# Kernel optimization log

Hardware: AMD Instinct MI355X
Metric: run time of the kernel (lower is better)

Reference implementation:

```python
import jax, jax.numpy as jnp
import numpy as np

PAD, CLS, SEP, UNK = 0, 1, 2, 3
VOCAB, DIM, LATENT = 30000, 768, 5000
B, L, C = 16, 1024, 8


def setup_inputs() -> dict:
    key = jax.random.key(0)
    k1, k2, k3 = jax.random.split(key, 3)
    x = jax.random.randint(k1, (B, L, C), 0, VOCAB, dtype=jnp.int64)
    char_emb = jax.random.normal(k2, (VOCAB, DIM), dtype=jnp.float32)
    latent_mat = jax.random.normal(k3, (LATENT, DIM), dtype=jnp.float32) * (LATENT ** -0.5)
    return {"x": x, "char_emb": char_emb, "latent_mat": latent_mat}


def reference(x, char_emb, latent_mat):
    b, l, c = x.shape
    chars = x.reshape(-1, c)                       # (N, C)
    embs = char_emb[chars]                         # (N, C, D) gather
    pad_mask = chars == PAD                        # (N, C)
    embs = jnp.where(pad_mask[..., None], 0.0, embs)
    summed = embs.sum(axis=1)                      # (N, D)
    counts = jnp.clip((~pad_mask).sum(axis=-1), 1, None)  # (N,)
    lang_emb = jnp.tanh(summed / counts[:, None].astype(summed.dtype))  # (N, D)

    # soft codebook attention: matmul -> softmax -> matmul
    scores = jnp.einsum('nd,kd->nk', lang_emb, latent_mat)   # (N, LATENT)
    dist = jax.nn.softmax(scores, axis=-1)
    latent_emb = jnp.einsum('nk,kd->nd', dist, latent_mat)    # (N, D)
    sde = lang_emb + latent_emb

    # special-token overwrite based on first char id
    first = chars[:, 0]
    for tid in (PAD, UNK, SEP, CLS):
        sde = jnp.where((first == tid)[:, None], char_emb[tid], sde)
    return sde.reshape(b, l, -1)
```

## Files before the change

### kernel.cpp

```cpp
#include <hip/hip_runtime.h>

#define PAD_ID 0
#define NTOK   16384
#define DIM    768
#define KLAT   5000
#define KPAD   5024
#define NSTEP  157
#define TILE_SH 24576
#define TOKB   64

typedef float f32x4 __attribute__((ext_vector_type(4)));
typedef __bf16 bf16x8 __attribute__((ext_vector_type(8)));

__device__ __forceinline__ unsigned int f2bf(float f) {
    unsigned int u = __float_as_uint(f);
    u += 0x7fffu + ((u >> 16) & 1u);
    return u >> 16;
}
__device__ __forceinline__ float bf2f(unsigned short h) {
    return __uint_as_float(((unsigned int)h) << 16);
}
__device__ __forceinline__ void async_cp16(const unsigned short* g, unsigned short* l) {
    __builtin_amdgcn_global_load_lds(
        (const __attribute__((address_space(1))) unsigned int*)g,
        (__attribute__((address_space(3))) unsigned int*)l, 16, 0, 0);
}

__global__ __launch_bounds__(256) void cvt_latS(const float* __restrict__ latent,
                                                unsigned short* __restrict__ latbS) {
    int g = blockIdx.x * 256 + threadIdx.x;
    if (g >= NSTEP * 24 * 2 * 64) return;
    int lane = g & 63; int rest = g >> 6;
    int h = rest & 1;  int kfr = rest >> 1;
    int kf = kfr % 24; int t  = kfr / 24;
    int row = t * 32 + h * 16 + (lane & 15);
    int col = kf * 32 + (lane >> 4) * 8;
    float4 v0 = make_float4(0.f,0.f,0.f,0.f), v1 = v0;
    if (row < KLAT) {
        v0 = *(const float4*)(latent + (long)row * DIM + col);
        v1 = *(const float4*)(latent + (long)row * DIM + col + 4);
    }
    uint4 o;
    o.x = f2bf(v0.x) | (f2bf(v0.y) << 16);
    o.y = f2bf(v0.z) | (f2bf(v0.w) << 16);
    o.z = f2bf(v1.x) | (f2bf(v1.y) << 16);
    o.w = f2bf(v1.z) | (f2bf(v1.w) << 16);
    *(uint4*)(latbS + (size_t)g * 8) = o;
}

__global__ __launch_bounds__(256) void cvt_latT(const float* __restrict__ latent,
                                                unsigned short* __restrict__ latbT) {
    int g = blockIdx.x * 256 + threadIdx.x;
    if (g >= NSTEP * DIM * 4) return;
    int kk8 = g & 3; int rest = g >> 2;
    int d = rest % DIM; int t = rest / DIM;
    int kk0 = kk8 * 8;
    unsigned short v[8];
    #pragma unroll
    for (int j = 0; j < 8; ++j) {
        int row = t * 32 + kk0 + j;
        v[j] = (row < KLAT) ? (unsigned short)f2bf(latent[(long)row * DIM + d])
                            : (unsigned short)0;
    }
    *(uint4*)(latbT + (size_t)g * 8) = *(uint4*)v;
}

__global__ __launch_bounds__(192) void build_lang(const int* __restrict__ x,
                                                  const float* __restrict__ cemb,
                                                  unsigned short* __restrict__ langb) {
    int tok = blockIdx.x;
    int t = threadIdx.x;
    const int* xs = x + tok * 8;
    int ids[8]; int cnt = 0;
    #pragma unroll
    for (int c = 0; c < 8; ++c) { ids[c] = xs[c]; cnt += (ids[c] != PAD_ID); }
    float4 acc = make_float4(0.f, 0.f, 0.f, 0.f);
    #pragma unroll
    for (int c = 0; c < 8; ++c) {
        if (ids[c] != PAD_ID) {
            float4 v = *(const float4*)(cemb + (long)ids[c] * DIM + t * 4);
            acc.x += v.x; acc.y += v.y; acc.z += v.z; acc.w += v.w;
        }
    }
    float cntf = (float)max(cnt, 1);
    unsigned int u0 = f2bf(tanhf(acc.x / cntf)) | (f2bf(tanhf(acc.y / cntf)) << 16);
    unsigned int u1 = f2bf(tanhf(acc.z / cntf)) | (f2bf(tanhf(acc.w / cntf)) << 16);
    *(uint2*)(langb + tok * DIM + t * 4) = make_uint2(u0, u1);
}

__global__ __launch_bounds__(512, 2) void fused_sde(
        const int* __restrict__ x, const float* __restrict__ cemb,
        const unsigned short* __restrict__ langb,
        const unsigned short* __restrict__ latbS,
        const unsigned short* __restrict__ latbT,
        float* __restrict__ out) {
    __shared__ unsigned short sLat[2][TILE_SH];
    __shared__ unsigned short sP[2][TOKB * 40];
    __shared__ float sL[2][TOKB];

    const int tid  = threadIdx.x;
    const int w    = tid >> 6;
    const int lane = tid & 63;
    const int lr   = lane & 15;
    const int q    = lane >> 4;
    const int tt   = w & 3;
    const int lt   = w >> 2;
    const int m0   = blockIdx.x * TOKB;

    uint4 qf[24];
    {
        const unsigned short* qr = langb + (m0 + tt * 16 + lr) * DIM;
        #pragma unroll
        for (int kf = 0; kf < 24; ++kf)
            qf[kf] = *(const uint4*)(qr + kf * 32 + q * 8);
    }

    f32x4 accO[4][6];
    #pragma unroll
    for (int mt = 0; mt < 4; ++mt)
        #pragma unroll
        for (int dt = 0; dt < 6; ++dt)
            accO[mt][dt] = (f32x4){0.f, 0.f, 0.f, 0.f};
    float lpart = 0.f;

    const int aBase = lt * 64 + lane;
    const int bBase = (w * 96 + lr) * 32 + q * 8;

    #pragma unroll
    for (int i = 0; i < 6; ++i)
        async_cp16(latbS + ((size_t)i * 512 + tid) * 8,
                   &sLat[0][(i * 512 + (tid & ~63)) * 8]);
    __syncthreads();

    for (int s = 0; s < NSTEP; ++s) {
        const int c = s & 1;

        {
            int nt = (s + 1 < NSTEP) ? s + 1 : 0;
            const unsigned short* gs = latbS + (size_t)nt * TILE_SH;
            #pragma unroll
            for (int i = 0; i < 6; ++i)
                async_cp16(gs + ((size_t)i * 512 + tid) * 8,
                           &sLat[c ^ 1][(i * 512 + (tid & ~63)) * 8]);
        }

        const unsigned short* bt = latbT + (size_t)s * TILE_SH;
        uint4 bO0[3], bO1[3];
        #pragma unroll
        for (int dt = 0; dt < 3; ++dt)
            bO0[dt] = *(const uint4*)(bt + bBase + dt * 512);

        f32x4 sva = {0.f,0.f,0.f,0.f}, svb = {0.f,0.f,0.f,0.f};
        #pragma unroll
        for (int kp = 0; kp < 12; ++kp) {
            bf16x8 a0 = *(const bf16x8*)&sLat[c][((2 * kp)     * 128 + aBase) * 8];
            bf16x8 a1 = *(const bf16x8*)&sLat[c][((2 * kp + 1) * 128 + aBase) * 8];
            bf16x8 b0 = *(const bf16x8*)&qf[2 * kp];
            bf16x8 b1 = *(const bf16x8*)&qf[2 * kp + 1];
            sva = __builtin_amdgcn_mfma_f32_16x16x32_bf16(a0, b0, sva, 0, 0, 0);
            svb = __builtin_amdgcn_mfma_f32_16x16x32_bf16(a1, b1, svb, 0, 0, 0);
        }

        #pragma unroll
        for (int dt = 0; dt < 3; ++dt)
            bO1[dt] = *(const uint4*)(bt + bBase + (dt + 3) * 512);

        {
            const int lat0 = s * 32 + lt * 16 + q * 4;
            f32x4 sv = sva + svb;
            float e0 = (lat0     < KLAT) ? __expf(sv[0]) : 0.f;
            float e1 = (lat0 + 1 < KLAT) ? __expf(sv[1]) : 0.f;
            float e2 = (lat0 + 2 < KLAT) ? __expf(sv[2]) : 0.f;
            float e3 = (lat0 + 3 < KLAT) ? __expf(sv[3]) : 0.f;
            lpart += (e0 + e1) + (e2 + e3);
            unsigned int p01 = f2bf(e0) | (f2bf(e1) << 16);
            unsigned int p23 = f2bf(e2) | (f2bf(e3) << 16);
            *(uint2*)&sP[c][(tt * 16 + lr) * 40 + lt * 16 + q * 4] =
                make_uint2(p01, p23);
        }

        __syncthreads();

        bf16x8 pA[4];
        #pragma unroll
        for (int mt = 0; mt < 4; ++mt)
            pA[mt] = *(const bf16x8*)&sP[c][(mt * 16 + lr) * 40 + q * 8];
        #pragma unroll
        for (int dt = 0; dt < 3; ++dt) {
            bf16x8 b = *(const bf16x8*)&bO0[dt];
            #pragma unroll
            for (int mt = 0; mt < 4; ++mt)
                accO[mt][dt] = __builtin_amdgcn_mfma_f32_16x16x32_bf16(
                    pA[mt], b, accO[mt][dt], 0, 0, 0);
        }
        #pragma unroll
        for (int dt = 0; dt < 3; ++dt) {
            bf16x8 b = *(const bf16x8*)&bO1[dt];
            #pragma unroll
            for (int mt = 0; mt < 4; ++mt)
                accO[mt][dt + 3] = __builtin_amdgcn_mfma_f32_16x16x32_bf16(
                    pA[mt], b, accO[mt][dt + 3], 0, 0, 0);
        }
    }

    lpart += __shfl_xor(lpart, 16, 64);
    lpart += __shfl_xor(lpart, 32, 64);
    if (lane < 16) sL[lt][tt * 16 + lane] = lpart;
    __syncthreads();

    #pragma unroll
    for (int mt = 0; mt < 4; ++mt) {
        int tl0 = mt * 16 + q * 4;
        float linv[4]; int fid[4];
        #pragma unroll
        for (int r = 0; r < 4; ++r) {
            linv[r] = 1.0f / (sL[0][tl0 + r] + sL[1][tl0 + r]);
            fid[r]  = x[(m0 + tl0 + r) * 8];
        }
        #pragma unroll
        for (int dt = 0; dt < 6; ++dt) {
            int d = w * 96 + dt * 16 + lr;
            #pragma unroll
            for (int r = 0; r < 4; ++r) {
                int tok = m0 + tl0 + r;
                float v = accO[mt][dt][r] * linv[r] + bf2f(langb[tok * DIM + d]);
                if (fid[r] < 4) v = cemb[fid[r] * DIM + d];
                out[tok * DIM + d] = v;
            }
        }
    }
}

extern "C" void kernel_launch(void* const* d_in, const int* in_sizes, int n_in,
                              void* d_out, int out_size, void* d_ws, size_t ws_size,
                              hipStream_t stream) {
    const int*   x      = (const int*)d_in[0];
    const float* cemb   = (const float*)d_in[1];
    const float* latent = (const float*)d_in[2];
    float* out = (float*)d_out;

    unsigned short* langb = (unsigned short*)d_ws;
    unsigned short* latbS = langb + (size_t)NTOK * DIM;
    unsigned short* latbT = latbS + (size_t)NSTEP * TILE_SH;

    int nS = NSTEP * 24 * 2 * 64;
    int nT = NSTEP * DIM * 4;
    cvt_latS<<<(nS + 255) / 256, 256, 0, stream>>>(latent, latbS);
    cvt_latT<<<(nT + 255) / 256, 256, 0, stream>>>(latent, latbT);
    build_lang<<<NTOK, 192, 0, stream>>>(x, cemb, langb);
    fused_sde<<<NTOK / TOKB, 512, 0, stream>>>(x, cemb, langb, latbS, latbT, out);
}
```

Before: 582.8 us.

## Split-K 32x32 score MFMA and software-pipeline PV matmul across steps

The score GEMM moves from 16x16x32 MFMAs to 32x32x16 MFMAs, with the K dimension split across four wave pairs and partial sums reduced through shared memory behind a lighter LDS-only barrier. The latS layout is reorganised to match the new fragment shape. The loop is software-pipelined so the P·V MFMAs of the previous step run in two halves interleaved with the current step's score computation, with s_setprio raising priority on the MFMA bursts. This aims to hide softmax/exp latency and barrier stalls behind matrix work, at the cost of extra LDS traffic for the cross-wave reduction and more complex synchronisation.

```diff
diff --git a/kernel.cpp b/kernel.cpp
--- a/kernel.cpp
+++ b/kernel.cpp
@@ -4,12 +4,12 @@
 #define NTOK   16384
 #define DIM    768
 #define KLAT   5000
-#define KPAD   5024
 #define NSTEP  157
 #define TILE_SH 24576
 #define TOKB   64
 
-typedef float f32x4 __attribute__((ext_vector_type(4)));
+typedef float  f32x4  __attribute__((ext_vector_type(4)));
+typedef float  f32x16 __attribute__((ext_vector_type(16)));
 typedef __bf16 bf16x8 __attribute__((ext_vector_type(8)));
 
 __device__ __forceinline__ unsigned int f2bf(float f) {
@@ -25,16 +25,21 @@
         (const __attribute__((address_space(1))) unsigned int*)g,
         (__attribute__((address_space(3))) unsigned int*)l, 16, 0, 0);
 }
+__device__ __forceinline__ void barrier_mid() {
+    asm volatile("s_waitcnt lgkmcnt(0)" ::: "memory");
+    __builtin_amdgcn_sched_barrier(0);
+    __builtin_amdgcn_s_barrier();
+    __builtin_amdgcn_sched_barrier(0);
+}
 
 __global__ __launch_bounds__(256) void cvt_latS(const float* __restrict__ latent,
                                                 unsigned short* __restrict__ latbS) {
     int g = blockIdx.x * 256 + threadIdx.x;
-    if (g >= NSTEP * 24 * 2 * 64) return;
+    if (g >= NSTEP * 48 * 64) return;
     int lane = g & 63; int rest = g >> 6;
-    int h = rest & 1;  int kfr = rest >> 1;
-    int kf = kfr % 24; int t  = kfr / 24;
-    int row = t * 32 + h * 16 + (lane & 15);
-    int col = kf * 32 + (lane >> 4) * 8;
+    int kb = rest % 48; int t = rest / 48;
+    int row = t * 32 + (lane & 31);
+    int col = kb * 16 + (lane >> 5) * 8;
     float4 v0 = make_float4(0.f,0.f,0.f,0.f), v1 = v0;
     if (row < KLAT) {
         v0 = *(const float4*)(latent + (long)row * DIM + col);
@@ -95,24 +100,28 @@
         const unsigned short* __restrict__ latbT,
         float* __restrict__ out) {
     __shared__ unsigned short sLat[2][TILE_SH];
-    __shared__ unsigned short sP[2][TOKB * 40];
-    __shared__ float sL[2][TOKB];
+    __shared__ unsigned short sPf[2][4 * 64 * 8];
+    __shared__ float pbuf[2][4][4][64][4];
+    __shared__ float sL[2][4][32];
 
     const int tid  = threadIdx.x;
     const int w    = tid >> 6;
     const int lane = tid & 63;
     const int lr   = lane & 15;
     const int q    = lane >> 4;
-    const int tt   = w & 3;
-    const int lt   = w >> 2;
+    const int l31  = lane & 31;
+    const int h    = lane >> 5;
+    const int tile = w & 1;
+    const int ks   = w >> 1;
     const int m0   = blockIdx.x * TOKB;
 
-    uint4 qf[24];
+    uint4 qf[12];
     {
-        const unsigned short* qr = langb + (m0 + tt * 16 + lr) * DIM;
-        #pragma unroll
-        for (int kf = 0; kf < 24; ++kf)
-            qf[kf] = *(const uint4*)(qr + kf * 32 + q * 8);
+        const unsigned short* qr =
+            langb + (size_t)(m0 + tile * 32 + l31) * DIM + ks * 192 + h * 8;
+        #pragma unroll
+        for (int kb = 0; kb < 12; ++kb)
+            qf[kb] = *(const uint4*)(qr + kb * 16);
     }
 
     f32x4 accO[4][6];
@@ -123,7 +132,7 @@
             accO[mt][dt] = (f32x4){0.f, 0.f, 0.f, 0.f};
     float lpart = 0.f;
 
-    const int aBase = lt * 64 + lane;
+    const int aBase = lane * 8;
     const int bBase = (w * 96 + lr) * 32 + q * 8;
 
     #pragma unroll
@@ -132,9 +141,47 @@
                    &sLat[0][(i * 512 + (tid & ~63)) * 8]);
     __syncthreads();
 
-    for (int s = 0; s < NSTEP; ++s) {
+    {
+        #pragma unroll
+        for (int i = 0; i < 6; ++i)
+            async_cp16(latbS + (size_t)TILE_SH + ((size_t)i * 512 + tid) * 8,
+                       &sLat[1][(i * 512 + (tid & ~63)) * 8]);
+        f32x16 sacc;
+        #pragma unroll
+        for (int i = 0; i < 16; ++i) sacc[i] = 0.f;
+        #pragma unroll
+        for (int kb = 0; kb < 12; ++kb) {
+            bf16x8 a = *(const bf16x8*)&sLat[0][(ks * 12 + kb) * 512 + aBase];
+            sacc = __builtin_amdgcn_mfma_f32_32x32x16_bf16(
+                a, *(const bf16x8*)&qf[kb], sacc, 0, 0, 0);
+        }
+        f32x4 own;
+        #pragma unroll
+        for (int g = 0; g < 4; ++g) {
+            f32x4 qv = {sacc[4*g+0], sacc[4*g+1], sacc[4*g+2], sacc[4*g+3]};
+            if (g == ks) own = qv;
+            else *(f32x4*)&pbuf[tile][ks][g][lane][0] = qv;
+        }
+        barrier_mid();
+        #pragma unroll
+        for (int p = 0; p < 4; ++p)
+            if (p != ks) own += *(const f32x4*)&pbuf[tile][p][ks][lane][0];
+        {
+            const int lat0 = 0 * 32 + ks * 8 + h * 4;
+            float e0 = (lat0     < KLAT) ? __expf(own[0]) : 0.f;
+            float e1 = (lat0 + 1 < KLAT) ? __expf(own[1]) : 0.f;
+            float e2 = (lat0 + 2 < KLAT) ? __expf(own[2]) : 0.f;
+            float e3 = (lat0 + 3 < KLAT) ? __expf(own[3]) : 0.f;
+            lpart += (e0 + e1) + (e2 + e3);
+            int mt = tile * 2 + (l31 >> 4);
+            *(uint2*)&sPf[0][(mt * 64 + lr + 16 * ks) * 8 + 4 * h] =
+                make_uint2(f2bf(e0) | (f2bf(e1) << 16), f2bf(e2) | (f2bf(e3) << 16));
+        }
+        __syncthreads();
+    }
+
+    for (int s = 1; s < NSTEP; ++s) {
         const int c = s & 1;
-
         {
             int nt = (s + 1 < NSTEP) ? s + 1 : 0;
             const unsigned short* gs = latbS + (size_t)nt * TILE_SH;
@@ -143,69 +190,93 @@
                 async_cp16(gs + ((size_t)i * 512 + tid) * 8,
                            &sLat[c ^ 1][(i * 512 + (tid & ~63)) * 8]);
         }
-
-        const unsigned short* bt = latbT + (size_t)s * TILE_SH;
-        uint4 bO0[3], bO1[3];
-        #pragma unroll
-        for (int dt = 0; dt < 3; ++dt)
-            bO0[dt] = *(const uint4*)(bt + bBase + dt * 512);
-
-        f32x4 sva = {0.f,0.f,0.f,0.f}, svb = {0.f,0.f,0.f,0.f};
-        #pragma unroll
-        for (int kp = 0; kp < 12; ++kp) {
-            bf16x8 a0 = *(const bf16x8*)&sLat[c][((2 * kp)     * 128 + aBase) * 8];
-            bf16x8 a1 = *(const bf16x8*)&sLat[c][((2 * kp + 1) * 128 + aBase) * 8];
-            bf16x8 b0 = *(const bf16x8*)&qf[2 * kp];
-            bf16x8 b1 = *(const bf16x8*)&qf[2 * kp + 1];
-            sva = __builtin_amdgcn_mfma_f32_16x16x32_bf16(a0, b0, sva, 0, 0, 0);
-            svb = __builtin_amdgcn_mfma_f32_16x16x32_bf16(a1, b1, svb, 0, 0, 0);
-        }
-
-        #pragma unroll
-        for (int dt = 0; dt < 3; ++dt)
-            bO1[dt] = *(const uint4*)(bt + bBase + (dt + 3) * 512);
-
+        const unsigned short* bt = latbT + (size_t)(s - 1) * TILE_SH;
+        uint4 bO[6];
+        #pragma unroll
+        for (int dt = 0; dt < 6; ++dt)
+            bO[dt] = *(const uint4*)(bt + bBase + dt * 512);
+        bf16x8 pA[4];
+        #pragma unroll
+        for (int mt = 0; mt < 4; ++mt)
+            pA[mt] = *(const bf16x8*)&sPf[c ^ 1][(mt * 64 + lane) * 8];
+
+        __builtin_amdgcn_s_setprio(1);
+        #pragma unroll
+        for (int dt = 0; dt < 6; ++dt) {
+            bf16x8 b = *(const bf16x8*)&bO[dt];
+            accO[0][dt] = __builtin_amdgcn_mfma_f32_16x16x32_bf16(pA[0], b, accO[0][dt], 0, 0, 0);
+            accO[1][dt] = __builtin_amdgcn_mfma_f32_16x16x32_bf16(pA[1], b, accO[1][dt], 0, 0, 0);
+        }
+        __builtin_amdgcn_s_setprio(0);
+
+        f32x16 sacc;
+        #pragma unroll
+        for (int i = 0; i < 16; ++i) sacc[i] = 0.f;
+        #pragma unroll
+        for (int kb = 0; kb < 12; ++kb) {
+            bf16x8 a = *(const bf16x8*)&sLat[c][(ks * 12 + kb) * 512 + aBase];
+            sacc = __builtin_amdgcn_mfma_f32_32x32x16_bf16(
+                a, *(const bf16x8*)&qf[kb], sacc, 0, 0, 0);
+        }
+        f32x4 own;
+        #pragma unroll
+        for (int g = 0; g < 4; ++g) {
+            f32x4 qv = {sacc[4*g+0], sacc[4*g+1], sacc[4*g+2], sacc[4*g+3]};
+            if (g == ks) own = qv;
+            else *(f32x4*)&pbuf[tile][ks][g][lane][0] = qv;
+        }
+
+        barrier_mid();
+
+        #pragma unroll
+        for (int p = 0; p < 4; ++p)
+            if (p != ks) own += *(const f32x4*)&pbuf[tile][p][ks][lane][0];
         {
-            const int lat0 = s * 32 + lt * 16 + q * 4;
-            f32x4 sv = sva + svb;
-            float e0 = (lat0     < KLAT) ? __expf(sv[0]) : 0.f;
-            float e1 = (lat0 + 1 < KLAT) ? __expf(sv[1]) : 0.f;
-            float e2 = (lat0 + 2 < KLAT) ? __expf(sv[2]) : 0.f;
-            float e3 = (lat0 + 3 < KLAT) ? __expf(sv[3]) : 0.f;
+            const int lat0 = s * 32 + ks * 8 + h * 4;
+            float e0 = (lat0     < KLAT) ? __expf(own[0]) : 0.f;
+            float e1 = (lat0 + 1 < KLAT) ? __expf(own[1]) : 0.f;
+            float e2 = (lat0 + 2 < KLAT) ? __expf(own[2]) : 0.f;
+            float e3 = (lat0 + 3 < KLAT) ? __expf(own[3]) : 0.f;
             lpart += (e0 + e1) + (e2 + e3);
-            unsigned int p01 = f2bf(e0) | (f2bf(e1) << 16);
-            unsigned int p23 = f2bf(e2) | (f2bf(e3) << 16);
-            *(uint2*)&sP[c][(tt * 16 + lr) * 40 + lt * 16 + q * 4] =
-                make_uint2(p01, p23);
-        }
+            int mt = tile * 2 + (l31 >> 4);
+            *(uint2*)&sPf[c][(mt * 64 + lr + 16 * ks) * 8 + 4 * h] =
+                make_uint2(f2bf(e0) | (f2bf(e1) << 16), f2bf(e2) | (f2bf(e3) << 16));
+        }
+
+        __builtin_amdgcn_s_setprio(1);
+        #pragma unroll
+        for (int dt = 0; dt < 6; ++dt) {
+            bf16x8 b = *(const bf16x8*)&bO[dt];
+            accO[2][dt] = __builtin_amdgcn_mfma_f32_16x16x32_bf16(pA[2], b, accO[2][dt], 0, 0, 0);
+            accO[3][dt] = __builtin_amdgcn_mfma_f32_16x16x32_bf16(pA[3], b, accO[3][dt], 0, 0, 0);
+        }
+        __builtin_amdgcn_s_setprio(0);
 
         __syncthreads();
-
+    }
+
+    {
+        const unsigned short* bt = latbT + (size_t)(NSTEP - 1) * TILE_SH;
+        uint4 bO[6];
+        #pragma unroll
+        for (int dt = 0; dt < 6; ++dt)
+            bO[dt] = *(const uint4*)(bt + bBase + dt * 512);
         bf16x8 pA[4];
         #pragma unroll
         for (int mt = 0; mt < 4; ++mt)
-            pA[mt] = *(const bf16x8*)&sP[c][(mt * 16 + lr) * 40 + q * 8];
-        #pragma unroll
-        for (int dt = 0; dt < 3; ++dt) {
-            bf16x8 b = *(const bf16x8*)&bO0[dt];
+            pA[mt] = *(const bf16x8*)&sPf[0][(mt * 64 + lane) * 8];
+        #pragma unroll
+        for (int dt = 0; dt < 6; ++dt) {
+            bf16x8 b = *(const bf16x8*)&bO[dt];
             #pragma unroll
             for (int mt = 0; mt < 4; ++mt)
                 accO[mt][dt] = __builtin_amdgcn_mfma_f32_16x16x32_bf16(
                     pA[mt], b, accO[mt][dt], 0, 0, 0);
         }
-        #pragma unroll
-        for (int dt = 0; dt < 3; ++dt) {
-            bf16x8 b = *(const bf16x8*)&bO1[dt];
-            #pragma unroll
-            for (int mt = 0; mt < 4; ++mt)
-                accO[mt][dt + 3] = __builtin_amdgcn_mfma_f32_16x16x32_bf16(
-                    pA[mt], b, accO[mt][dt + 3], 0, 0, 0);
-        }
-    }
-
-    lpart += __shfl_xor(lpart, 16, 64);
+    }
+
     lpart += __shfl_xor(lpart, 32, 64);
-    if (lane < 16) sL[lt][tt * 16 + lane] = lpart;
+    if (lane < 32) sL[tile][ks][lane] = lpart;
     __syncthreads();
 
     #pragma unroll
@@ -214,8 +285,11 @@
         float linv[4]; int fid[4];
         #pragma unroll
         for (int r = 0; r < 4; ++r) {
-            linv[r] = 1.0f / (sL[0][tl0 + r] + sL[1][tl0 + r]);
-            fid[r]  = x[(m0 + tl0 + r) * 8];
+            int tok = tl0 + r;
+            float den = sL[tok >> 5][0][tok & 31] + sL[tok >> 5][1][tok & 31] +
+                        sL[tok >> 5][2][tok & 31] + sL[tok >> 5][3][tok & 31];
+            linv[r] = 1.0f / den;
+            fid[r]  = x[(m0 + tok) * 8];
         }
         #pragma unroll
         for (int dt = 0; dt < 6; ++dt) {
@@ -243,7 +317,7 @@
     unsigned short* latbS = langb + (size_t)NTOK * DIM;
     unsigned short* latbT = latbS + (size_t)NSTEP * TILE_SH;
 
-    int nS = NSTEP * 24 * 2 * 64;
+    int nS = NSTEP * 48 * 64;
     int nT = NSTEP * DIM * 4;
     cvt_latS<<<(nS + 255) / 256, 256, 0, stream>>>(latent, latbS);
     cvt_latT<<<(nT + 255) / 256, 256, 0, stream>>>(latent, latbT);
```

Measured after the change: 582.6 us. Within noise of the previous version (-0.0%).

## Warp-specialize fused kernel into score/softmax and PV-accumulate warp groups

Applied to the files above, without the earlier changes.

Splits the 512-thread block into two 4-wave groups. One group computes QK scores and exp for a tile while the other runs the PV MFMA accumulation on the previous tile and issues the async latent prefetches. The two groups synchronize through a raw s_barrier helper with explicit waitcnt. This is meant to overlap the softmax/exp phase with the output matmul, but it doubles the accumulator registers per PV wave to 4x12 f32x4, which may hurt occupancy under launch_bounds(512,2). Barrier counts have to match exactly across both groups.

```diff
diff --git a/kernel.cpp b/kernel.cpp
--- a/kernel.cpp
+++ b/kernel.cpp
@@ -4,7 +4,6 @@
 #define NTOK   16384
 #define DIM    768
 #define KLAT   5000
-#define KPAD   5024
 #define NSTEP  157
 #define TILE_SH 24576
 #define TOKB   64
@@ -24,6 +23,12 @@
     __builtin_amdgcn_global_load_lds(
         (const __attribute__((address_space(1))) unsigned int*)g,
         (__attribute__((address_space(3))) unsigned int*)l, 16, 0, 0);
+}
+__device__ __forceinline__ void gang_bar() {
+    asm volatile("s_waitcnt vmcnt(0) lgkmcnt(0)" ::: "memory");
+    __builtin_amdgcn_sched_barrier(0);
+    __builtin_amdgcn_s_barrier();
+    __builtin_amdgcn_sched_barrier(0);
 }
 
 __global__ __launch_bounds__(256) void cvt_latS(const float* __restrict__ latent,
@@ -96,35 +101,14 @@
         float* __restrict__ out) {
     __shared__ unsigned short sLat[2][TILE_SH];
     __shared__ unsigned short sP[2][TOKB * 40];
-    __shared__ float sL[2][TOKB];
+    __shared__ float sL[TOKB];
 
     const int tid  = threadIdx.x;
     const int w    = tid >> 6;
     const int lane = tid & 63;
     const int lr   = lane & 15;
     const int q    = lane >> 4;
-    const int tt   = w & 3;
-    const int lt   = w >> 2;
     const int m0   = blockIdx.x * TOKB;
-
-    uint4 qf[24];
-    {
-        const unsigned short* qr = langb + (m0 + tt * 16 + lr) * DIM;
-        #pragma unroll
-        for (int kf = 0; kf < 24; ++kf)
-            qf[kf] = *(const uint4*)(qr + kf * 32 + q * 8);
-    }
-
-    f32x4 accO[4][6];
-    #pragma unroll
-    for (int mt = 0; mt < 4; ++mt)
-        #pragma unroll
-        for (int dt = 0; dt < 6; ++dt)
-            accO[mt][dt] = (f32x4){0.f, 0.f, 0.f, 0.f};
-    float lpart = 0.f;
-
-    const int aBase = lt * 64 + lane;
-    const int bBase = (w * 96 + lr) * 32 + q * 8;
 
     #pragma unroll
     for (int i = 0; i < 6; ++i)
@@ -132,100 +116,122 @@
                    &sLat[0][(i * 512 + (tid & ~63)) * 8]);
     __syncthreads();
 
-    for (int s = 0; s < NSTEP; ++s) {
-        const int c = s & 1;
-
+    if (w < 4) {
+        const int tt = w;
+        uint4 qf[24];
         {
-            int nt = (s + 1 < NSTEP) ? s + 1 : 0;
-            const unsigned short* gs = latbS + (size_t)nt * TILE_SH;
-            #pragma unroll
-            for (int i = 0; i < 6; ++i)
-                async_cp16(gs + ((size_t)i * 512 + tid) * 8,
-                           &sLat[c ^ 1][(i * 512 + (tid & ~63)) * 8]);
-        }
-
-        const unsigned short* bt = latbT + (size_t)s * TILE_SH;
-        uint4 bO0[3], bO1[3];
-        #pragma unroll
-        for (int dt = 0; dt < 3; ++dt)
-            bO0[dt] = *(const uint4*)(bt + bBase + dt * 512);
-
-        f32x4 sva = {0.f,0.f,0.f,0.f}, svb = {0.f,0.f,0.f,0.f};
-        #pragma unroll
-        for (int kp = 0; kp < 12; ++kp) {
-            bf16x8 a0 = *(const bf16x8*)&sLat[c][((2 * kp)     * 128 + aBase) * 8];
-            bf16x8 a1 = *(const bf16x8*)&sLat[c][((2 * kp + 1) * 128 + aBase) * 8];
-            bf16x8 b0 = *(const bf16x8*)&qf[2 * kp];
-            bf16x8 b1 = *(const bf16x8*)&qf[2 * kp + 1];
-            sva = __builtin_amdgcn_mfma_f32_16x16x32_bf16(a0, b0, sva, 0, 0, 0);
-            svb = __builtin_amdgcn_mfma_f32_16x16x32_bf16(a1, b1, svb, 0, 0, 0);
-        }
-
-        #pragma unroll
-        for (int dt = 0; dt < 3; ++dt)
-            bO1[dt] = *(const uint4*)(bt + bBase + (dt + 3) * 512);
-
-        {
-            const int lat0 = s * 32 + lt * 16 + q * 4;
-            f32x4 sv = sva + svb;
-            float e0 = (lat0     < KLAT) ? __expf(sv[0]) : 0.f;
-            float e1 = (lat0 + 1 < KLAT) ? __expf(sv[1]) : 0.f;
-            float e2 = (lat0 + 2 < KLAT) ? __expf(sv[2]) : 0.f;
-            float e3 = (lat0 + 3 < KLAT) ? __expf(sv[3]) : 0.f;
-            lpart += (e0 + e1) + (e2 + e3);
-            unsigned int p01 = f2bf(e0) | (f2bf(e1) << 16);
-            unsigned int p23 = f2bf(e2) | (f2bf(e3) << 16);
-            *(uint2*)&sP[c][(tt * 16 + lr) * 40 + lt * 16 + q * 4] =
-                make_uint2(p01, p23);
-        }
-
-        __syncthreads();
-
-        bf16x8 pA[4];
+            const unsigned short* qr = langb + (m0 + tt * 16 + lr) * DIM;
+            #pragma unroll
+            for (int kf = 0; kf < 24; ++kf)
+                qf[kf] = *(const uint4*)(qr + kf * 32 + q * 8);
+        }
+        float lpart = 0.f;
+
+        for (int p = 0; p < NSTEP; ++p) {
+            const int c = p & 1;
+            f32x4 sva0 = {0.f,0.f,0.f,0.f}, sva1 = {0.f,0.f,0.f,0.f};
+            f32x4 svb0 = {0.f,0.f,0.f,0.f}, svb1 = {0.f,0.f,0.f,0.f};
+            #pragma unroll
+            for (int kp = 0; kp < 12; ++kp) {
+                bf16x8 a00 = *(const bf16x8*)&sLat[c][((2*kp)   * 128 +      lane) * 8];
+                bf16x8 a01 = *(const bf16x8*)&sLat[c][((2*kp)   * 128 + 64 + lane) * 8];
+                bf16x8 a10 = *(const bf16x8*)&sLat[c][((2*kp+1) * 128 +      lane) * 8];
+                bf16x8 a11 = *(const bf16x8*)&sLat[c][((2*kp+1) * 128 + 64 + lane) * 8];
+                bf16x8 b0 = *(const bf16x8*)&qf[2*kp];
+                bf16x8 b1 = *(const bf16x8*)&qf[2*kp+1];
+                sva0 = __builtin_amdgcn_mfma_f32_16x16x32_bf16(a00, b0, sva0, 0, 0, 0);
+                sva1 = __builtin_amdgcn_mfma_f32_16x16x32_bf16(a01, b0, sva1, 0, 0, 0);
+                svb0 = __builtin_amdgcn_mfma_f32_16x16x32_bf16(a10, b1, svb0, 0, 0, 0);
+                svb1 = __builtin_amdgcn_mfma_f32_16x16x32_bf16(a11, b1, svb1, 0, 0, 0);
+            }
+            {
+                const int lat0 = p * 32 + q * 4;
+                f32x4 sv0 = sva0 + svb0;
+                f32x4 sv1 = sva1 + svb1;
+                float e0 = (lat0      < KLAT) ? __expf(sv0[0]) : 0.f;
+                float e1 = (lat0 + 1  < KLAT) ? __expf(sv0[1]) : 0.f;
+                float e2 = (lat0 + 2  < KLAT) ? __expf(sv0[2]) : 0.f;
+                float e3 = (lat0 + 3  < KLAT) ? __expf(sv0[3]) : 0.f;
+                float f0 = (lat0 + 16 < KLAT) ? __expf(sv1[0]) : 0.f;
+                float f1 = (lat0 + 17 < KLAT) ? __expf(sv1[1]) : 0.f;
+                float f2 = (lat0 + 18 < KLAT) ? __expf(sv1[2]) : 0.f;
+                float f3 = (lat0 + 19 < KLAT) ? __expf(sv1[3]) : 0.f;
+                lpart += (e0 + e1) + (e2 + e3) + (f0 + f1) + (f2 + f3);
+                unsigned short* prow = &sP[c][(tt * 16 + lr) * 40];
+                *(uint2*)&prow[q * 4] =
+                    make_uint2(f2bf(e0) | (f2bf(e1) << 16), f2bf(e2) | (f2bf(e3) << 16));
+                *(uint2*)&prow[16 + q * 4] =
+                    make_uint2(f2bf(f0) | (f2bf(f1) << 16), f2bf(f2) | (f2bf(f3) << 16));
+            }
+            gang_bar();
+        }
+        lpart += __shfl_xor(lpart, 16, 64);
+        lpart += __shfl_xor(lpart, 32, 64);
+        if (lane < 16) sL[tt * 16 + lane] = lpart;
+        gang_bar();
+    } else {
+        const int wb = w - 4;
+        const int tb = tid - 256;
+        const int bBase = (wb * 192 + lr) * 32 + q * 8;
+        f32x4 accO[4][12];
         #pragma unroll
         for (int mt = 0; mt < 4; ++mt)
-            pA[mt] = *(const bf16x8*)&sP[c][(mt * 16 + lr) * 40 + q * 8];
+            #pragma unroll
+            for (int dt = 0; dt < 12; ++dt)
+                accO[mt][dt] = (f32x4){0.f, 0.f, 0.f, 0.f};
+
+        for (int p = 0; p <= NSTEP; ++p) {
+            const int c = p & 1;
+            if (p < NSTEP - 1) {
+                const unsigned short* gs = latbS + (size_t)(p + 1) * TILE_SH;
+                #pragma unroll
+                for (int i = 0; i < 12; ++i)
+                    async_cp16(gs + ((size_t)(i * 256 + tb)) * 8,
+                               &sLat[c ^ 1][(i * 256 + (tb & ~63)) * 8]);
+            }
+            if (p > 0) {
+                const unsigned short* bt = latbT + (size_t)(p - 1) * TILE_SH;
+                bf16x8 pA[4];
+                #pragma unroll
+                for (int mt = 0; mt < 4; ++mt)
+                    pA[mt] = *(const bf16x8*)&sP[c ^ 1][(mt * 16 + lr) * 40 + q * 8];
+                #pragma unroll
+                for (int r3 = 0; r3 < 3; ++r3) {
+                    uint4 bO[4];
+                    #pragma unroll
+                    for (int j = 0; j < 4; ++j)
+                        bO[j] = *(const uint4*)(bt + bBase + (r3 * 4 + j) * 512);
+                    #pragma unroll
+                    for (int j = 0; j < 4; ++j) {
+                        bf16x8 b = *(const bf16x8*)&bO[j];
+                        #pragma unroll
+                        for (int mt = 0; mt < 4; ++mt)
+                            accO[mt][r3 * 4 + j] = __builtin_amdgcn_mfma_f32_16x16x32_bf16(
+                                pA[mt], b, accO[mt][r3 * 4 + j], 0, 0, 0);
+                    }
+                }
+            }
+            gang_bar();
+        }
         #pragma unroll
-        for (int dt = 0; dt < 3; ++dt) {
-            bf16x8 b = *(const bf16x8*)&bO0[dt];
-            #pragma unroll
-            for (int mt = 0; mt < 4; ++mt)
-                accO[mt][dt] = __builtin_amdgcn_mfma_f32_16x16x32_bf16(
-                    pA[mt], b, accO[mt][dt], 0, 0, 0);
-        }
-        #pragma unroll
-        for (int dt = 0; dt < 3; ++dt) {
-            bf16x8 b = *(const bf16x8*)&bO1[dt];
-            #pragma unroll
-            for (int mt = 0; mt < 4; ++mt)
-                accO[mt][dt + 3] = __builtin_amdgcn_mfma_f32_16x16x32_bf16(
-                    pA[mt], b, accO[mt][dt + 3], 0, 0, 0);
-        }
-    }
-
-    lpart += __shfl_xor(lpart, 16, 64);
-    lpart += __shfl_xor(lpart, 32, 64);
-    if (lane < 16) sL[lt][tt * 16 + lane] = lpart;
-    __syncthreads();
-
-    #pragma unroll
-    for (int mt = 0; mt < 4; ++mt) {
-        int tl0 = mt * 16 + q * 4;
-        float linv[4]; int fid[4];
-        #pragma unroll
-        for (int r = 0; r < 4; ++r) {
-            linv[r] = 1.0f / (sL[0][tl0 + r] + sL[1][tl0 + r]);
-            fid[r]  = x[(m0 + tl0 + r) * 8];
-        }
-        #pragma unroll
-        for (int dt = 0; dt < 6; ++dt) {
-            int d = w * 96 + dt * 16 + lr;
+        for (int mt = 0; mt < 4; ++mt) {
+            int tl0 = mt * 16 + q * 4;
+            float linv[4]; int fid[4];
             #pragma unroll
             for (int r = 0; r < 4; ++r) {
-                int tok = m0 + tl0 + r;
-                float v = accO[mt][dt][r] * linv[r] + bf2f(langb[tok * DIM + d]);
-                if (fid[r] < 4) v = cemb[fid[r] * DIM + d];
-                out[tok * DIM + d] = v;
+                linv[r] = 1.0f / sL[tl0 + r];
+                fid[r]  = x[(m0 + tl0 + r) * 8];
+            }
+            #pragma unroll
+            for (int dt = 0; dt < 12; ++dt) {
+                int d = wb * 192 + dt * 16 + lr;
+                #pragma unroll
+                for (int r = 0; r < 4; ++r) {
+                    int tok = m0 + tl0 + r;
+                    float v = accO[mt][dt][r] * linv[r] + bf2f(langb[tok * DIM + d]);
+                    if (fid[r] < 4) v = cemb[fid[r] * DIM + d];
+                    out[tok * DIM + d] = v;
+                }
             }
         }
     }
```

Measured after the change: 614.2 us. 1.05x slower.

## Triple-buffer latent tiles and software-pipeline PV matmul one step behind

Applied to the files above, without the earlier changes.

Moves from double to triple buffering of the latent score tiles, so loads run two steps ahead. The P·V matmul for step s-1 is issued during step s, with a single barrier per iteration, explicit vmcnt waits and sched barriers. MFMA priority is raised around the PV block. Launch bounds drop to one block per SIMD pair to allow more registers and LDS, which trades away occupancy.

```diff
diff --git a/kernel.cpp b/kernel.cpp
--- a/kernel.cpp
+++ b/kernel.cpp
@@ -4,7 +4,6 @@
 #define NTOK   16384
 #define DIM    768
 #define KLAT   5000
-#define KPAD   5024
 #define NSTEP  157
 #define TILE_SH 24576
 #define TOKB   64
@@ -88,13 +87,13 @@
     *(uint2*)(langb + tok * DIM + t * 4) = make_uint2(u0, u1);
 }
 
-__global__ __launch_bounds__(512, 2) void fused_sde(
+__global__ __launch_bounds__(512, 1) void fused_sde(
         const int* __restrict__ x, const float* __restrict__ cemb,
         const unsigned short* __restrict__ langb,
         const unsigned short* __restrict__ latbS,
         const unsigned short* __restrict__ latbT,
         float* __restrict__ out) {
-    __shared__ unsigned short sLat[2][TILE_SH];
+    __shared__ unsigned short sLat[3][TILE_SH];
     __shared__ unsigned short sP[2][TOKB * 40];
     __shared__ float sL[2][TOKB];
 
@@ -130,40 +129,50 @@
     for (int i = 0; i < 6; ++i)
         async_cp16(latbS + ((size_t)i * 512 + tid) * 8,
                    &sLat[0][(i * 512 + (tid & ~63)) * 8]);
-    __syncthreads();
+    __builtin_amdgcn_sched_barrier(0);
+    #pragma unroll
+    for (int i = 0; i < 6; ++i)
+        async_cp16(latbS + (size_t)TILE_SH + ((size_t)i * 512 + tid) * 8,
+                   &sLat[1][(i * 512 + (tid & ~63)) * 8]);
+    __builtin_amdgcn_sched_barrier(0);
+    asm volatile("s_waitcnt vmcnt(6)" ::: "memory");
+    __builtin_amdgcn_sched_barrier(0);
+    __builtin_amdgcn_s_barrier();
+    __builtin_amdgcn_sched_barrier(0);
+
+    uint4 bO[6];
 
     for (int s = 0; s < NSTEP; ++s) {
-        const int c = s & 1;
-
-        {
-            int nt = (s + 1 < NSTEP) ? s + 1 : 0;
-            const unsigned short* gs = latbS + (size_t)nt * TILE_SH;
+        const int c  = s & 1;
+        const int rb = s % 3;
+
+        if (s > 0) {
+            const unsigned short* bt = latbT + (size_t)(s - 1) * TILE_SH;
+            #pragma unroll
+            for (int dt = 0; dt < 6; ++dt)
+                bO[dt] = *(const uint4*)(bt + bBase + dt * 512);
+        }
+        __builtin_amdgcn_sched_barrier(0);
+        if (s + 2 < NSTEP) {
+            const unsigned short* gs = latbS + (size_t)(s + 2) * TILE_SH;
+            const int rn = (s + 2) % 3;
             #pragma unroll
             for (int i = 0; i < 6; ++i)
                 async_cp16(gs + ((size_t)i * 512 + tid) * 8,
-                           &sLat[c ^ 1][(i * 512 + (tid & ~63)) * 8]);
-        }
-
-        const unsigned short* bt = latbT + (size_t)s * TILE_SH;
-        uint4 bO0[3], bO1[3];
-        #pragma unroll
-        for (int dt = 0; dt < 3; ++dt)
-            bO0[dt] = *(const uint4*)(bt + bBase + dt * 512);
+                           &sLat[rn][(i * 512 + (tid & ~63)) * 8]);
+        }
+        __builtin_amdgcn_sched_barrier(0);
 
         f32x4 sva = {0.f,0.f,0.f,0.f}, svb = {0.f,0.f,0.f,0.f};
         #pragma unroll
         for (int kp = 0; kp < 12; ++kp) {
-            bf16x8 a0 = *(const bf16x8*)&sLat[c][((2 * kp)     * 128 + aBase) * 8];
-            bf16x8 a1 = *(const bf16x8*)&sLat[c][((2 * kp + 1) * 128 + aBase) * 8];
+            bf16x8 a0 = *(const bf16x8*)&sLat[rb][((2 * kp)     * 128 + aBase) * 8];
+            bf16x8 a1 = *(const bf16x8*)&sLat[rb][((2 * kp + 1) * 128 + aBase) * 8];
             bf16x8 b0 = *(const bf16x8*)&qf[2 * kp];
             bf16x8 b1 = *(const bf16x8*)&qf[2 * kp + 1];
             sva = __builtin_amdgcn_mfma_f32_16x16x32_bf16(a0, b0, sva, 0, 0, 0);
             svb = __builtin_amdgcn_mfma_f32_16x16x32_bf16(a1, b1, svb, 0, 0, 0);
         }
-
-        #pragma unroll
-        for (int dt = 0; dt < 3; ++dt)
-            bO1[dt] = *(const uint4*)(bt + bBase + (dt + 3) * 512);
 
         {
             const int lat0 = s * 32 + lt * 16 + q * 4;
@@ -179,27 +188,52 @@
                 make_uint2(p01, p23);
         }
 
-        __syncthreads();
-
+        if (s + 2 < NSTEP) {
+            asm volatile("s_waitcnt vmcnt(6)" ::: "memory");
+        } else {
+            asm volatile("s_waitcnt vmcnt(0)" ::: "memory");
+        }
+        __builtin_amdgcn_sched_barrier(0);
+
+        if (s > 0) {
+            bf16x8 pA[4];
+            #pragma unroll
+            for (int mt = 0; mt < 4; ++mt)
+                pA[mt] = *(const bf16x8*)&sP[c ^ 1][(mt * 16 + lr) * 40 + q * 8];
+            __builtin_amdgcn_s_setprio(1);
+            #pragma unroll
+            for (int dt = 0; dt < 6; ++dt) {
+                bf16x8 b = *(const bf16x8*)&bO[dt];
+                #pragma unroll
+                for (int mt = 0; mt < 4; ++mt)
+                    accO[mt][dt] = __builtin_amdgcn_mfma_f32_16x16x32_bf16(
+                        pA[mt], b, accO[mt][dt], 0, 0, 0);
+            }
+            __builtin_amdgcn_s_setprio(0);
+        }
+
+        asm volatile("s_waitcnt lgkmcnt(0)" ::: "memory");
+        __builtin_amdgcn_sched_barrier(0);
+        __builtin_amdgcn_s_barrier();
+        __builtin_amdgcn_sched_barrier(0);
+    }
+
+    {
+        const unsigned short* bt = latbT + (size_t)(NSTEP - 1) * TILE_SH;
+        #pragma unroll
+        for (int dt = 0; dt < 6; ++dt)
+            bO[dt] = *(const uint4*)(bt + bBase + dt * 512);
         bf16x8 pA[4];
         #pragma unroll
         for (int mt = 0; mt < 4; ++mt)
-            pA[mt] = *(const bf16x8*)&sP[c][(mt * 16 + lr) * 40 + q * 8];
-        #pragma unroll
-        for (int dt = 0; dt < 3; ++dt) {
-            bf16x8 b = *(const bf16x8*)&bO0[dt];
+            pA[mt] = *(const bf16x8*)&sP[0][(mt * 16 + lr) * 40 + q * 8];
+        #pragma unroll
+        for (int dt = 0; dt < 6; ++dt) {
+            bf16x8 b = *(const bf16x8*)&bO[dt];
             #pragma unroll
             for (int mt = 0; mt < 4; ++mt)
                 accO[mt][dt] = __builtin_amdgcn_mfma_f32_16x16x32_bf16(
                     pA[mt], b, accO[mt][dt], 0, 0, 0);
-        }
-        #pragma unroll
-        for (int dt = 0; dt < 3; ++dt) {
-            bf16x8 b = *(const bf16x8*)&bO1[dt];
-            #pragma unroll
-            for (int mt = 0; mt < 4; ++mt)
-                accO[mt][dt + 3] = __builtin_amdgcn_mfma_f32_16x16x32_bf16(
-                    pA[mt], b, accO[mt][dt + 3], 0, 0, 0);
         }
     }
 
```

Result: faster. 555.0 us (-4.8%).
